# Optimization experiments

Measured on AMD Instinct MI355X. Metric: run time of the kernel, lower is better.

## Reference

```python
import jax, jax.numpy as jnp
import numpy as np

B, S, V, D = 4, 128, 50257, 1024

def setup_inputs() -> dict:
    key = jax.random.key(0)
    k1, k2 = jax.random.split(key)
    # pred_probs: a probability simplex over vocab per (b, s); module initializes
    # to uniform by default, we use normalized uniform noise for a non-degenerate test.
    p = jax.random.uniform(k1, (B, S, V), dtype=jnp.float32) + 1e-3
    pred_probs = p / jnp.sum(p, axis=-1, keepdims=True)
    embed_weight = jax.random.normal(k2, (V, D), dtype=jnp.float32) * 0.02
    return {"pred_probs": pred_probs, "embed_weight": embed_weight}

def reference(pred_probs, embed_weight):
    # do_sample=False, st=False default path of TargetProbability.forward_multiple
    # predictions: argmax over vocab
    predictions = jnp.argmax(pred_probs, axis=-1)  # [B, S] int
    # soft embedding: (pred_probs.unsqueeze(-1) * embed_lut.weight).sum(-2)
    # == GEMM over the vocab dim, avoiding the [B,S,V,D] intermediate.
    pred_emb = jnp.einsum('bsv,vd->bsd', pred_probs, embed_weight)  # [B, S, D]
    return pred_emb, predictions, pred_probs
```

## Files before the change

### kernel.cpp

```cpp
#include <hip/hip_runtime.h>

#define MROWS 512
#define VDIM  50257
#define KP    50304
#define NDIM  1024
#define NST32 1572
#define KSPLIT 32
#define SC     50
#define PRED_OFF 524288
#define PP_OFF   524800
#define NPREP  4096
#define CHUNK  6288
#define NCONVW 12576

typedef unsigned short u16;
typedef unsigned int   u32;
typedef unsigned long long u64;
typedef __bf16 bf16x8 __attribute__((ext_vector_type(8)));
typedef u16    u16x8  __attribute__((ext_vector_type(8)));
typedef float  f32x4  __attribute__((ext_vector_type(4)));
typedef float  f32x4u __attribute__((ext_vector_type(4), aligned(4)));

__device__ __forceinline__ u16 f2bf(float f) {
  u32 u = __float_as_uint(f);
  u32 r = (u + 0x7fffu + ((u >> 16) & 1u)) >> 16;
  return (u16)r;
}

__device__ __forceinline__ void gl_lds16(const u16* g, u16* l) {
  __builtin_amdgcn_global_load_lds(
      (const __attribute__((address_space(1))) u32*)(g),
      (__attribute__((address_space(3))) u32*)(l), 16, 0, 0);
}

__global__ __launch_bounds__(256) void prep_kernel(const float* __restrict__ P,
                                                   float* __restrict__ out,
                                                   u16* __restrict__ A,
                                                   u64* __restrict__ amax)
{
  const int tid = threadIdx.x;
  const int bx  = blockIdx.x;
  const int m  = bx >> 3;
  const int c  = bx & 7;
  const int s0 = c * CHUNK;
  const int len = min(VDIM - s0, CHUNK);
  const float* row = P + (size_t)m * VDIM;
  float*       crw = out + PP_OFF + (size_t)m * VDIM;
  u16*        arow = A + (size_t)m * KP;

  if (tid < 32) { f32x4 z = {}; *(f32x4*)(out + (size_t)m * NDIM + c * 128 + tid * 4) = z; }

  u64 best = 0;
#define TRK(val, idx) do { \
    u64 pk = ((u64)__float_as_uint(val) << 32) | (u64)(0xFFFFu - (u32)(idx)); \
    best = best > pk ? best : pk; } while (0)
#define GRP(cc) do {                                                     \
    f32x4u va = *(const f32x4u*)(row + (cc));                            \
    f32x4u vb = *(const f32x4u*)(row + (cc) + 4);                        \
    *(f32x4u*)(crw + (cc))     = va;                                     \
    *(f32x4u*)(crw + (cc) + 4) = vb;                                     \
    u16x8 o;                                                             \
    o[0]=f2bf(va[0]); o[1]=f2bf(va[1]); o[2]=f2bf(va[2]); o[3]=f2bf(va[3]); \
    o[4]=f2bf(vb[0]); o[5]=f2bf(vb[1]); o[6]=f2bf(vb[2]); o[7]=f2bf(vb[3]); \
    *(u16x8*)(arow + (cc)) = o;                                          \
    TRK(va[0],(cc)); TRK(va[1],(cc)+1); TRK(va[2],(cc)+2); TRK(va[3],(cc)+3); \
    TRK(vb[0],(cc)+4); TRK(vb[1],(cc)+5); TRK(vb[2],(cc)+6); TRK(vb[3],(cc)+7); \
  } while (0)

  const int ng = len >> 3;
  int i = tid;
  for (; i + 256 < ng; i += 512) {
    const int c0 = s0 + (i << 3);
    const int c1 = c0 + 2048;
    GRP(c0);
    GRP(c1);
  }
  if (i < ng) GRP(s0 + (i << 3));
  if (tid < (len & 7)) {
    const int col = s0 + (ng << 3) + tid;
    float v = row[col];
    crw[col] = v;
    arow[col] = f2bf(v);
    TRK(v, col);
  }
#undef GRP
#undef TRK
  if (c == 7 && tid < KP - VDIM) arow[VDIM + tid] = 0;

  __shared__ u64 sb[256];
  sb[tid] = best;
  __syncthreads();
  for (int s = 128; s > 0; s >>= 1) {
    if (tid < s) { u64 o = sb[tid + s]; if (o > sb[tid]) sb[tid] = o; }
    __syncthreads();
  }
  if (tid == 0) atomicMax(&amax[m], sb[0]);
}

__global__ __launch_bounds__(256) void convw_kernel(const float* __restrict__ W,
                                                    u16* __restrict__ BT)
{
  const int cidx = blockIdx.x;
  __shared__ u16 t[64][72];
  const int tid = threadIdx.x;
  const int dt  = cidx & 15;
  const int vt  = cidx >> 4;
  const int v0  = vt << 6;
  const int d0  = dt << 6;
  const int c16 = tid & 15;
  const int r16 = tid >> 4;
#pragma unroll
  for (int p = 0; p < 4; ++p) {
    const int v  = v0 + p * 16 + r16;
    const int vl = p * 16 + r16;
    float4 w = make_float4(0.f, 0.f, 0.f, 0.f);
    if (v < VDIM) w = *(const float4*)(W + (size_t)v * NDIM + d0 + c16 * 4);
    t[c16 * 4 + 0][vl] = f2bf(w.x);
    t[c16 * 4 + 1][vl] = f2bf(w.y);
    t[c16 * 4 + 2][vl] = f2bf(w.z);
    t[c16 * 4 + 3][vl] = f2bf(w.w);
  }
  __syncthreads();
#pragma unroll
  for (int p = 0; p < 2; ++p) {
    const int dl = p * 32 + (tid >> 3);
    const int vl = (tid & 7) * 8;
    u16x8 o = *(const u16x8*)(&t[dl][vl]);
    *(u16x8*)(BT + (size_t)(d0 + dl) * KP + v0 + vl) = o;
  }
}

__global__ __launch_bounds__(512, 1) void gemm_kernel(const u16* __restrict__ A,
                                                      const u16* __restrict__ BT,
                                                      const u64* __restrict__ amax,
                                                      float* __restrict__ out)
{
  __shared__ u16 ldsA[4][256 * 32];
  __shared__ u16 ldsB[4][256 * 32];

  const int bx  = blockIdx.x;
  const int kc  = (bx & 7) | ((bx >> 6) << 3);
  const int mn  = (bx >> 3) & 7;
  const int m0  = (mn & 1) << 8;
  const int n0  = (mn >> 1) << 8;
  const int ks0 = kc * SC;
  const int ks1 = min(NST32, ks0 + SC);
  const int tid  = threadIdx.x;
  const int wid  = tid >> 6;
  const int lane = tid & 63;
  const int wr   = wid >> 2;
  const int wc   = wid & 3;

  if (bx == 0) {
    u64 p = amax[tid];
    out[PRED_OFF + tid] = (float)(0xFFFF - (int)(p & 0xFFFFu));
  }

  const int sp  = lane >> 3;
  const int sx  = (lane & 7) ^ sp;
  const int srow = 2 * sp + (sx >> 2);
  const int skel = (sx & 3) << 3;
  const u16* gA = A  + (size_t)(m0 + wid * 32 + srow) * KP + skel;
  const u16* gB = BT + (size_t)(n0 + wid * 32 + srow) * KP + skel;

  f32x4 acc[8][4] = {};

  const int r   = lane & 15;
  const int q4  = lane >> 4;
  const int sl  = (((r & 1) << 2) | q4) ^ ((r >> 1) & 7);
  const int rb2A = (wr * 128 + (r & ~1)) * 32 + sl * 8;
  const int rb2B = (wc * 64  + (r & ~1)) * 32 + sl * 8;

#define STAGE(buf, ks) do {                                              \
    const size_t k_ = (size_t)(ks) << 5;                                 \
    gl_lds16(gA + k_,                 &ldsA[buf][(wid * 32) * 32]);      \
    gl_lds16(gA + k_ + (size_t)16*KP, &ldsA[buf][(wid * 32 + 16) * 32]); \
    gl_lds16(gB + k_,                 &ldsB[buf][(wid * 32) * 32]);      \
    gl_lds16(gB + k_ + (size_t)16*KP, &ldsB[buf][(wid * 32 + 16) * 32]); \
  } while (0)

  STAGE(0, ks0);
  if (ks0 + 1 < ks1) STAGE(1, ks0 + 1);
  if (ks0 + 2 < ks1) STAGE(2, ks0 + 2);

  int b = 0;
  for (int ks = ks0; ks < ks1; ++ks) {
    if (ks + 2 < ks1)      asm volatile("s_waitcnt vmcnt(8) lgkmcnt(0)" ::: "memory");
    else if (ks + 1 < ks1) asm volatile("s_waitcnt vmcnt(4) lgkmcnt(0)" ::: "memory");
    else                   asm volatile("s_waitcnt vmcnt(0) lgkmcnt(0)" ::: "memory");
    __builtin_amdgcn_s_barrier();
    if (ks + 3 < ks1) STAGE((b + 3) & 3, ks + 3);

    const u16* lA = ldsA[b];
    const u16* lB = ldsB[b];
    bf16x8 av[8], bv[4];
#pragma unroll
    for (int i = 0; i < 8; ++i) av[i] = *(const bf16x8*)(lA + rb2A + i * 512);
#pragma unroll
    for (int j = 0; j < 4; ++j) bv[j] = *(const bf16x8*)(lB + rb2B + j * 512);

    __builtin_amdgcn_s_setprio(1);
#pragma unroll
    for (int i = 0; i < 8; ++i)
#pragma unroll
      for (int j = 0; j < 4; ++j)
        acc[i][j] = __builtin_amdgcn_mfma_f32_16x16x32_bf16(av[i], bv[j], acc[i][j], 0, 0, 0);
    __builtin_amdgcn_s_setprio(0);
    __builtin_amdgcn_sched_barrier(0);
    b = (b + 1) & 3;
  }
#undef STAGE

  const int col = lane & 15;
  const int r4  = q4 << 2;
#pragma unroll
  for (int i = 0; i < 8; ++i)
#pragma unroll
    for (int j = 0; j < 4; ++j)
#pragma unroll
      for (int rr = 0; rr < 4; ++rr) {
        const int mm = m0 + wr * 128 + i * 16 + r4 + rr;
        const int nn = n0 + wc * 64 + j * 16 + col;
        atomicAdd(out + (size_t)mm * NDIM + nn, acc[i][j][rr]);
      }
}

extern "C" void kernel_launch(void* const* d_in, const int* in_sizes, int n_in,
                              void* d_out, int out_size, void* d_ws, size_t ws_size,
                              hipStream_t stream) {
  const float* P = (const float*)d_in[0];
  const float* W = (const float*)d_in[1];
  float* out = (float*)d_out;
  u64* amax = (u64*)d_ws;
  u16* A  = (u16*)((char*)d_ws + 4096);
  u16* BT = A + (size_t)MROWS * KP;

  hipMemsetAsync(amax, 0, MROWS * sizeof(u64), stream);
  prep_kernel<<<NPREP, 256, 0, stream>>>(P, out, A, amax);
  convw_kernel<<<NCONVW, 256, 0, stream>>>(W, BT);
  gemm_kernel<<<256, 512, 0, stream>>>(A, BT, amax, out);
}
```

Baseline: 239.0 us.

## Shrink GEMM tiles to 128x128 with 1024 blocks and add two-stage split-K reduction

The GEMM moves from 256x256 tiles with 512 threads and 4-stage LDS buffering to 128x128 tiles with 256 threads, double buffering and up to 4 blocks per CU, launching 1024 blocks for better occupancy. Split-K partials can now be written to a workspace buffer and summed by a separate reduce kernel instead of using float atomics. The reduce kernel fully overwrites the output tile, so the zeroing in prep becomes redundant on that path. The smaller tiles lower operand reuse, the shallower pipeline may expose more latency, and the 64MB partial buffer adds DRAM traffic plus an extra launch. The two-stage path is used only when the workspace is large enough, otherwise the kernel falls back to atomics.

```diff
diff --git a/kernel.cpp b/kernel.cpp
--- a/kernel.cpp
+++ b/kernel.cpp
@@ -6,7 +6,6 @@
 #define NDIM  1024
 #define NST32 1572
 #define KSPLIT 32
-#define SC     50
 #define PRED_OFF 524288
 #define PP_OFF   524800
 #define NPREP  4096
@@ -130,46 +129,54 @@
   }
 }
 
-__global__ __launch_bounds__(512, 1) void gemm_kernel(const u16* __restrict__ A,
+template <int TS>
+__global__ __launch_bounds__(256, 4) void gemm_kernel(const u16* __restrict__ A,
                                                       const u16* __restrict__ BT,
                                                       const u64* __restrict__ amax,
-                                                      float* __restrict__ out)
-{
-  __shared__ u16 ldsA[4][256 * 32];
-  __shared__ u16 ldsB[4][256 * 32];
+                                                      float* __restrict__ out,
+                                                      float* __restrict__ Pp)
+{
+  __shared__ u16 ldsA[2][128 * 32];
+  __shared__ u16 ldsB[2][128 * 32];
 
   const int bx  = blockIdx.x;
-  const int kc  = (bx & 7) | ((bx >> 6) << 3);
-  const int mn  = (bx >> 3) & 7;
-  const int m0  = (mn & 1) << 8;
-  const int n0  = (mn >> 1) << 8;
-  const int ks0 = kc * SC;
-  const int ks1 = min(NST32, ks0 + SC);
+  const int x   = bx & 7;
+  const int s   = bx >> 3;
+  const int kc  = x + ((s >> 5) << 3);
+  const int mn  = s & 31;
+  const int mt  = mn & 3;
+  const int nt  = mn >> 2;
+  const int m0  = mt << 7;
+  const int n0  = nt << 7;
+  const int ks0 = (kc * NST32) / KSPLIT;
+  const int ks1 = ((kc + 1) * NST32) / KSPLIT;
   const int tid  = threadIdx.x;
   const int wid  = tid >> 6;
   const int lane = tid & 63;
-  const int wr   = wid >> 2;
-  const int wc   = wid & 3;
+  const int wr   = wid >> 1;
+  const int wc   = wid & 1;
 
   if (bx == 0) {
-    u64 p = amax[tid];
-    out[PRED_OFF + tid] = (float)(0xFFFF - (int)(p & 0xFFFFu));
-  }
-
-  const int sp  = lane >> 3;
-  const int sx  = (lane & 7) ^ sp;
+    u64 p0 = amax[tid];
+    u64 p1 = amax[tid + 256];
+    out[PRED_OFF + tid]       = (float)(0xFFFF - (int)(p0 & 0xFFFFu));
+    out[PRED_OFF + tid + 256] = (float)(0xFFFF - (int)(p1 & 0xFFFFu));
+  }
+
+  const int sp   = lane >> 3;
+  const int sx   = (lane & 7) ^ sp;
   const int srow = 2 * sp + (sx >> 2);
   const int skel = (sx & 3) << 3;
   const u16* gA = A  + (size_t)(m0 + wid * 32 + srow) * KP + skel;
   const u16* gB = BT + (size_t)(n0 + wid * 32 + srow) * KP + skel;
 
-  f32x4 acc[8][4] = {};
+  f32x4 acc[4][4] = {};
 
   const int r   = lane & 15;
   const int q4  = lane >> 4;
   const int sl  = (((r & 1) << 2) | q4) ^ ((r >> 1) & 7);
-  const int rb2A = (wr * 128 + (r & ~1)) * 32 + sl * 8;
-  const int rb2B = (wc * 64  + (r & ~1)) * 32 + sl * 8;
+  const int rb2A = (wr * 64 + (r & ~1)) * 32 + sl * 8;
+  const int rb2B = (wc * 64 + (r & ~1)) * 32 + sl * 8;
 
 #define STAGE(buf, ks) do {                                              \
     const size_t k_ = (size_t)(ks) << 5;                                 \
@@ -180,49 +187,79 @@
   } while (0)
 
   STAGE(0, ks0);
-  if (ks0 + 1 < ks1) STAGE(1, ks0 + 1);
-  if (ks0 + 2 < ks1) STAGE(2, ks0 + 2);
 
   int b = 0;
   for (int ks = ks0; ks < ks1; ++ks) {
-    if (ks + 2 < ks1)      asm volatile("s_waitcnt vmcnt(8) lgkmcnt(0)" ::: "memory");
-    else if (ks + 1 < ks1) asm volatile("s_waitcnt vmcnt(4) lgkmcnt(0)" ::: "memory");
-    else                   asm volatile("s_waitcnt vmcnt(0) lgkmcnt(0)" ::: "memory");
+    asm volatile("s_waitcnt vmcnt(0)" ::: "memory");
     __builtin_amdgcn_s_barrier();
-    if (ks + 3 < ks1) STAGE((b + 3) & 3, ks + 3);
+    if (ks + 1 < ks1) STAGE(b ^ 1, ks + 1);
 
     const u16* lA = ldsA[b];
     const u16* lB = ldsB[b];
-    bf16x8 av[8], bv[4];
-#pragma unroll
-    for (int i = 0; i < 8; ++i) av[i] = *(const bf16x8*)(lA + rb2A + i * 512);
+    bf16x8 av[4], bv[4];
+#pragma unroll
+    for (int i = 0; i < 4; ++i) av[i] = *(const bf16x8*)(lA + rb2A + i * 512);
 #pragma unroll
     for (int j = 0; j < 4; ++j) bv[j] = *(const bf16x8*)(lB + rb2B + j * 512);
 
     __builtin_amdgcn_s_setprio(1);
 #pragma unroll
-    for (int i = 0; i < 8; ++i)
+    for (int i = 0; i < 4; ++i)
 #pragma unroll
       for (int j = 0; j < 4; ++j)
         acc[i][j] = __builtin_amdgcn_mfma_f32_16x16x32_bf16(av[i], bv[j], acc[i][j], 0, 0, 0);
     __builtin_amdgcn_s_setprio(0);
     __builtin_amdgcn_sched_barrier(0);
-    b = (b + 1) & 3;
+    b ^= 1;
   }
 #undef STAGE
 
   const int col = lane & 15;
-  const int r4  = q4 << 2;
-#pragma unroll
-  for (int i = 0; i < 8; ++i)
-#pragma unroll
-    for (int j = 0; j < 4; ++j)
-#pragma unroll
-      for (int rr = 0; rr < 4; ++rr) {
-        const int mm = m0 + wr * 128 + i * 16 + r4 + rr;
-        const int nn = n0 + wc * 64 + j * 16 + col;
-        atomicAdd(out + (size_t)mm * NDIM + nn, acc[i][j][rr]);
-      }
+  if (TS) {
+    float* pp = Pp + (size_t)bx * 16384;
+#pragma unroll
+    for (int i = 0; i < 4; ++i)
+#pragma unroll
+      for (int j = 0; j < 4; ++j)
+#pragma unroll
+        for (int rr = 0; rr < 4; ++rr) {
+          const int mm = wr * 64 + i * 16 + q4 * 4 + rr;
+          const int nn = wc * 64 + j * 16 + col;
+          pp[mm * 128 + nn] = acc[i][j][rr];
+        }
+  } else {
+#pragma unroll
+    for (int i = 0; i < 4; ++i)
+#pragma unroll
+      for (int j = 0; j < 4; ++j)
+#pragma unroll
+        for (int rr = 0; rr < 4; ++rr) {
+          const int mm = m0 + wr * 64 + i * 16 + q4 * 4 + rr;
+          const int nn = n0 + wc * 64 + j * 16 + col;
+          atomicAdd(out + (size_t)mm * NDIM + nn, acc[i][j][rr]);
+        }
+  }
+}
+
+__global__ __launch_bounds__(256) void reduce_kernel(const float* __restrict__ Pp,
+                                                     float* __restrict__ out)
+{
+  const int t   = blockIdx.x * 256 + threadIdx.x;
+  const int m   = t >> 8;
+  const int n0q = (t & 255) << 2;
+  const int mt  = m >> 7;
+  const int nt  = n0q >> 7;
+  const size_t base = (size_t)(m & 127) * 128 + (n0q & 127);
+
+  f32x4 sacc[4] = {};
+#pragma unroll
+  for (int kc = 0; kc < 32; ++kc) {
+    const int bxp = (((kc >> 3) * 32 + (nt << 2) + mt) << 3) + (kc & 7);
+    f32x4 v = *(const f32x4*)(Pp + (size_t)bxp * 16384 + base);
+    sacc[kc & 3] += v;
+  }
+  f32x4 rsum = (sacc[0] + sacc[1]) + (sacc[2] + sacc[3]);
+  *(f32x4*)(out + (size_t)m * NDIM + n0q) = rsum;
 }
 
 extern "C" void kernel_launch(void* const* d_in, const int* in_sizes, int n_in,
@@ -234,9 +271,18 @@
   u64* amax = (u64*)d_ws;
   u16* A  = (u16*)((char*)d_ws + 4096);
   u16* BT = A + (size_t)MROWS * KP;
+  const size_t pp_off = 4096 + (size_t)MROWS * KP * 2 + (size_t)NDIM * KP * 2;
+  const size_t pp_bytes = (size_t)1024 * 16384 * 4;
+  float* Pp = (float*)((char*)d_ws + pp_off);
+  const bool two_stage = (ws_size >= pp_off + pp_bytes);
 
   hipMemsetAsync(amax, 0, MROWS * sizeof(u64), stream);
   prep_kernel<<<NPREP, 256, 0, stream>>>(P, out, A, amax);
   convw_kernel<<<NCONVW, 256, 0, stream>>>(W, BT);
-  gemm_kernel<<<256, 512, 0, stream>>>(A, BT, amax, out);
-}
+  if (two_stage) {
+    gemm_kernel<1><<<1024, 256, 0, stream>>>(A, BT, amax, out, Pp);
+    reduce_kernel<<<512, 256, 0, stream>>>(Pp, out);
+  } else {
+    gemm_kernel<0><<<1024, 256, 0, stream>>>(A, BT, amax, out, Pp);
+  }
+}
```

Result: faster. 217.9 us (-8.9%).
